# Kernel tuning notes

Measured on AMD Instinct MI355X. Metric: run time of the kernel, lower is better.

## Reference

```python
import jax, jax.numpy as jnp
import numpy as np

N_HEAD = 16


def setup_inputs() -> dict:
    key = jax.random.key(0)
    ks = jax.random.split(key, 5)
    B, T, C = 2, 2048, 1024
    s = 1.0 / np.sqrt(C)
    inp = {
        "x": jax.random.normal(ks[0], (B, T, C), dtype=jnp.float32),
        "Wq": jax.random.normal(ks[1], (C, C), dtype=jnp.float32) * s,
        "bq": jnp.zeros((C,), dtype=jnp.float32),
        "Wk": jax.random.normal(ks[2], (C, C), dtype=jnp.float32) * s,
        "bk": jnp.zeros((C,), dtype=jnp.float32),
        "Wv": jax.random.normal(ks[3], (C, C), dtype=jnp.float32) * s,
        "bv": jnp.zeros((C,), dtype=jnp.float32),
        "Wp": jax.random.normal(ks[4], (C, C), dtype=jnp.float32) * s,
        "bp": jnp.zeros((C,), dtype=jnp.float32),
    }
    return inp


def reference(x, Wq, bq, Wk, bk, Wv, bv, Wp, bp):
    B, T, C = x.shape
    H = N_HEAD
    D = C // H
    # linear projections (torch Linear: x @ W.T + b)
    q = (x @ Wq.T + bq).reshape(B, T, H, D)
    k = (x @ Wk.T + bk).reshape(B, T, H, D)
    v = (x @ Wv.T + bv).reshape(B, T, H, D)
    # scaled dot-product attention (NO causal mask in original forward)
    att = jnp.einsum("bthd,bshd->bhts", q, k) * (1.0 / np.sqrt(D))
    att = jax.nn.softmax(att, axis=-1)
    y = jnp.einsum("bhts,bshd->bthd", att, v).reshape(B, T, C)
    # output projection (dropouts are identity at p=0 / eval)
    return y @ Wp.T + bp
```

## Files before the change

### kernel.cpp

```cpp
#include <hip/hip_runtime.h>
#include <hip/hip_bf16.h>

typedef __attribute__((ext_vector_type(4))) float f32x4;
typedef __attribute__((ext_vector_type(16))) float f32x16;
typedef __attribute__((ext_vector_type(8))) short bf16x8;
typedef __attribute__((ext_vector_type(2))) unsigned int u32x2;

#define T_SEQ 2048
#define C_DIM 1024
#define NH 16
#define DHD 64

__device__ __forceinline__ unsigned cvtpk_bf16(float lo, float hi) {
    unsigned r;
    asm("v_cvt_pk_bf16_f32 %0, %1, %2" : "=v"(r) : "v"(lo), "v"(hi));
    return r;
}

__device__ __forceinline__ void async_copy16(void* lds, const void* g) {
    __builtin_amdgcn_global_load_lds(
        (const __attribute__((address_space(1))) unsigned int*)(uintptr_t)g,
        (__attribute__((address_space(3))) unsigned int*)(unsigned int)(uintptr_t)lds,
        16, 0, 0);
}

__global__ __launch_bounds__(256) void cvt_all(const float* __restrict__ x,
                                               const float* __restrict__ Wq, const float* __restrict__ Wk,
                                               const float* __restrict__ Wv, const float* __restrict__ Wp,
                                               __hip_bfloat16* __restrict__ xb,
                                               __hip_bfloat16* __restrict__ wf,
                                               __hip_bfloat16* __restrict__ wpb) {
    int i = blockIdx.x * blockDim.x + threadIdx.x;
    const float* src; __hip_bfloat16* dst; int off;
    if (i < 1048576) { src = x; dst = xb; off = i; }
    else {
        int j = i - 1048576; int wi = j >> 18; off = j & 262143;
        switch (wi) {
            case 0:  src = Wq; dst = wf;           break;
            case 1:  src = Wk; dst = wf + 1048576; break;
            case 2:  src = Wv; dst = wf + 2097152; break;
            default: src = Wp; dst = wpb;          break;
        }
    }
    float4 v = *(const float4*)(src + (size_t)off * 4);
    __hip_bfloat16 h0 = __float2bfloat16(v.x), h1 = __float2bfloat16(v.y);
    __hip_bfloat16 h2 = __float2bfloat16(v.z), h3 = __float2bfloat16(v.w);
    union { __hip_bfloat16 h[4]; u32x2 u; } p;
    p.h[0] = h0; p.h[1] = h1; p.h[2] = h2; p.h[3] = h3;
    *(u32x2*)(dst + (size_t)off * 4) = p.u;
}

__global__ __launch_bounds__(512) void gemm_qkv(const __hip_bfloat16* __restrict__ A,
                                                const __hip_bfloat16* __restrict__ Bw,
                                                const float* __restrict__ biasq,
                                                const float* __restrict__ biask,
                                                const float* __restrict__ biasv,
                                                __hip_bfloat16* __restrict__ oq,
                                                __hip_bfloat16* __restrict__ okk,
                                                __hip_bfloat16* __restrict__ ovt) {
    __shared__ __align__(16) char lds[131072];

    const int xcd = (int)blockIdx.x & 7, loc = (int)blockIdx.x >> 3;
    const int mloc = loc / 6, nloc = loc - mloc * 6;
    const int m0 = ((xcd & 3) * 4 + mloc) * 256;
    const int n0 = ((xcd >> 2) * 6 + nloc) * 256;

    const int tid = threadIdx.x;
    const int w = tid >> 6, l = tid & 63;
    const int wr = w >> 2, wc = w & 3;
    const int lg = l >> 4, lr = l & 15;

    const int sr0 = tid >> 3;
    const int sc0 = (tid & 7) * 16;
    const int gc0 = sc0 ^ ((sr0 & 7) << 4);
    const size_t goff = (size_t)sr0 * 2048 + gc0;

    const char* Ag = (const char*)A + (size_t)m0 * 2048;
    const char* Bg = (const char*)Bw + (size_t)n0 * 2048;

    auto STAGE_A = [&](int buf, int half, int kt) {
        const char* g = Ag + (size_t)(half * 128) * 2048 + kt * 128 + goff;
        char* d = lds + (buf * 2 + half) * 16384 + w * 1024;
        async_copy16(d, g);
        async_copy16(d + 8192, g + (size_t)64 * 2048);
    };
    auto STAGE_B = [&](int buf, int half, int kt) {
        const char* g = Bg + (size_t)(half * 128) * 2048 + kt * 128 + goff;
        char* d = lds + 65536 + (buf * 2 + half) * 16384 + w * 1024;
        async_copy16(d, g);
        async_copy16(d + 8192, g + (size_t)64 * 2048);
    };

    const int sw = (lr & 7) << 4;
    auto LDA = [&](bf16x8* af, int buf, int mq) {
        const char* base = lds + (buf * 2 + wr) * 16384;
        #pragma unroll
        for (int m = 0; m < 4; m++) {
            const int r = (mq * 4 + m) * 16 + lr;
            #pragma unroll
            for (int kk = 0; kk < 2; kk++)
                af[m * 2 + kk] = *(const bf16x8*)(base + r * 128 + ((kk * 64 + lg * 16) ^ sw));
        }
    };
    auto LDB = [&](bf16x8* bfv, int buf, int nq) {
        const char* base = lds + 65536 + (buf * 2 + (wc >> 1)) * 16384;
        #pragma unroll
        for (int n = 0; n < 2; n++) {
            const int r = (wc & 1) * 64 + (nq * 2 + n) * 16 + lr;
            #pragma unroll
            for (int kk = 0; kk < 2; kk++)
                bfv[n * 2 + kk] = *(const bf16x8*)(base + r * 128 + ((kk * 64 + lg * 16) ^ sw));
        }
    };

    f32x4 acc[8][4] = {};
    auto MF = [&](const bf16x8* af, const bf16x8* bfv, int mq, int nq) {
        #pragma unroll
        for (int m = 0; m < 4; m++)
            #pragma unroll
            for (int n = 0; n < 2; n++)
                #pragma unroll
                for (int kk = 0; kk < 2; kk++)
                    acc[mq * 4 + m][nq * 2 + n] = __builtin_amdgcn_mfma_f32_16x16x32_bf16(
                        af[m * 2 + kk], bfv[n * 2 + kk], acc[mq * 4 + m][nq * 2 + n], 0, 0, 0);
    };

#define PH_OPEN()  __builtin_amdgcn_sched_barrier(0); \
                   __builtin_amdgcn_s_barrier(); \
                   asm volatile("s_waitcnt lgkmcnt(0)" ::: "memory"); \
                   __builtin_amdgcn_sched_barrier(0); \
                   __builtin_amdgcn_s_setprio(1);
#define PH_CLOSE() __builtin_amdgcn_s_setprio(0); \
                   __builtin_amdgcn_sched_barrier(0); \
                   __builtin_amdgcn_s_barrier();
#define PH_CLOSE_VM() __builtin_amdgcn_s_setprio(0); \
                   asm volatile("s_waitcnt vmcnt(6)" ::: "memory"); \
                   __builtin_amdgcn_sched_barrier(0); \
                   __builtin_amdgcn_s_barrier();

    bf16x8 af[8], bf0[4], bf1[4];

    STAGE_B(0, 0, 0); STAGE_B(0, 1, 0); STAGE_A(0, 0, 0); STAGE_A(0, 1, 0);
    STAGE_B(1, 0, 1); STAGE_B(1, 1, 1); STAGE_A(1, 0, 1);
    asm volatile("s_waitcnt vmcnt(6)" ::: "memory");
    __builtin_amdgcn_sched_barrier(0);
    __builtin_amdgcn_s_barrier();

    for (int it = 0; it < 8; ++it) {
        const int t1 = 2 * it + 1;
        const int c2 = (2 * it + 2 < 16) ? 2 * it + 2 : 14;
        const int c3 = (2 * it + 3 < 16) ? 2 * it + 3 : 15;
        const int b2 = c2 & 1, b3 = c3 & 1;

        LDA(af, 0, 0); LDB(bf0, 0, 0);
        STAGE_A(1, 1, t1);
        PH_OPEN(); MF(af, bf0, 0, 0); PH_CLOSE();
        LDB(bf1, 0, 1);
        PH_OPEN(); MF(af, bf1, 0, 1); PH_CLOSE();
        LDA(af, 0, 1);
        STAGE_B(b2, 0, c2);
        PH_OPEN(); MF(af, bf1, 1, 1); PH_CLOSE();
        STAGE_B(b2, 1, c2); STAGE_A(b2, 0, c2);
        PH_OPEN(); MF(af, bf0, 1, 0); PH_CLOSE_VM();

        LDA(af, 1, 0); LDB(bf0, 1, 0);
        STAGE_A(b2, 1, c2);
        PH_OPEN(); MF(af, bf0, 0, 0); PH_CLOSE();
        LDB(bf1, 1, 1);
        PH_OPEN(); MF(af, bf1, 0, 1); PH_CLOSE();
        LDA(af, 1, 1);
        STAGE_B(b3, 0, c3);
        PH_OPEN(); MF(af, bf1, 1, 1); PH_CLOSE();
        STAGE_B(b3, 1, c3); STAGE_A(b3, 0, c3);
        PH_OPEN(); MF(af, bf0, 1, 0); PH_CLOSE_VM();
    }
#undef PH_OPEN
#undef PH_CLOSE
#undef PH_CLOSE_VM

    const int proj = n0 >> 10;
    const float* bias = (proj == 0) ? biasq : (proj == 1) ? biask : biasv;
    const float bsc = (proj == 0) ? 0.125f : 1.0f;
    #pragma unroll
    for (int m = 0; m < 8; m++)
        #pragma unroll
        for (int n = 0; n < 4; n++)
            #pragma unroll
            for (int rr = 0; rr < 4; rr++) {
                int row = m0 + wr * 128 + m * 16 + lg * 4 + rr;
                int col = n0 + wc * 64 + n * 16 + lr;
                int colL = col & (C_DIM - 1);
                float val = (acc[m][n][rr] + bias[colL]) * bsc;
                int b = row >> 11, t = row & 2047, hh = colL >> 6, dd = colL & 63;
                if (proj < 2) {
                    __hip_bfloat16* dst = (proj == 0) ? oq : okk;
                    dst[(((size_t)(b * NH + hh)) * T_SEQ + t) * DHD + dd] = __float2bfloat16(val);
                } else {
                    ovt[(((size_t)(b * NH + hh)) * DHD + dd) * T_SEQ + t] = __float2bfloat16(val);
                }
            }
}

__global__ __launch_bounds__(256) void gemm_proj(const __hip_bfloat16* __restrict__ A,
                                                 const __hip_bfloat16* __restrict__ Bw,
                                                 const float* __restrict__ biasp,
                                                 float* __restrict__ outf) {
    __shared__ __align__(16) char As[128 * 128];
    __shared__ __align__(16) char Bs[128 * 128];

    const int nwg = gridDim.x;
    const int cpx = nwg >> 3;
    const int wg = ((int)blockIdx.x & 7) * cpx + ((int)blockIdx.x >> 3);
    const int m0 = (wg & 31) * 128;
    const int n0 = (wg >> 5) * 128;

    const int tid = threadIdx.x;
    const int w = tid >> 6, l = tid & 63;
    const int wr = w >> 1, wc = w & 1;
    const int lg = l >> 4, lr = l & 15;

    const char* Ag = (const char*)A + (size_t)m0 * 2048;
    const char* Bg = (const char*)Bw + (size_t)n0 * 2048;
    const int lrow = l >> 3;
    const int scol = (l & 7) * 16;

    f32x4 acc[4][4] = {};

    for (int kt = 0; kt < 16; ++kt) {
        __syncthreads();
        #pragma unroll
        for (int i = 0; i < 4; i++) {
            const int rb = w * 32 + i * 8;
            const size_t go = (size_t)(rb + lrow) * 2048 + (size_t)kt * 128 + scol;
            async_copy16(&As[rb * 128], Ag + go);
            async_copy16(&Bs[rb * 128], Bg + go);
        }
        __syncthreads();
        #pragma unroll
        for (int kk = 0; kk < 2; kk++) {
            bf16x8 af[4], bfr[4];
            #pragma unroll
            for (int m = 0; m < 4; m++)
                af[m] = *(const bf16x8*)(&As[(wr * 64 + m * 16 + lr) * 128 + kk * 64 + lg * 16]);
            #pragma unroll
            for (int n = 0; n < 4; n++)
                bfr[n] = *(const bf16x8*)(&Bs[(wc * 64 + n * 16 + lr) * 128 + kk * 64 + lg * 16]);
            #pragma unroll
            for (int m = 0; m < 4; m++)
                #pragma unroll
                for (int n = 0; n < 4; n++)
                    acc[m][n] = __builtin_amdgcn_mfma_f32_16x16x32_bf16(af[m], bfr[n], acc[m][n], 0, 0, 0);
        }
    }

    #pragma unroll
    for (int m = 0; m < 4; m++)
        #pragma unroll
        for (int n = 0; n < 4; n++)
            #pragma unroll
            for (int r = 0; r < 4; r++) {
                int row = m0 + wr * 64 + m * 16 + lg * 4 + r;
                int col = n0 + wc * 64 + n * 16 + lr;
                outf[(size_t)row * C_DIM + col] = acc[m][n][r] + biasp[col];
            }
}

__global__ __launch_bounds__(256) void attn4(const __hip_bfloat16* __restrict__ Q,
                                             const __hip_bfloat16* __restrict__ K,
                                             const __hip_bfloat16* __restrict__ Vt,
                                             __hip_bfloat16* __restrict__ Y) {
    const int bid = blockIdx.x;
    const int xcd = bid & 7, slot = bid >> 3;
    const int head = xcd * 4 + (slot & 3);
    const int qblk = slot >> 2;

    const int tid = threadIdx.x;
    const int w = tid >> 6, l = tid & 63;
    const int lq = l & 31, hi = l >> 5;
    const int q0 = qblk * 128 + w * 32;

    __shared__ __align__(16) char Ks[3][8192];
    __shared__ __align__(16) char Vs[3][8192];
    __shared__ float bc[4][32];

    const char* Kb = (const char*)(K + (size_t)head * T_SEQ * DHD);
    const char* Vb = (const char*)(Vt + (size_t)head * DHD * T_SEQ);

    bf16x8 qf[4];
    {
        const char* qrow = (const char*)(Q + ((size_t)head * T_SEQ + q0 + lq) * DHD);
        #pragma unroll
        for (int t = 0; t < 4; t++) qf[t] = *(const bf16x8*)(qrow + t * 32 + hi * 16);
    }

    f32x16 yacc[2] = {};
    float ls0 = 0.f, ls1 = 0.f, ls2 = 0.f, ls3 = 0.f;

    const int o0 = (2 * w) * 1024 + l * 16;
    const int o1 = o0 + 1024;
    const int r0 = o0 >> 7, c0b = o0 & 127;
    const int r1 = o1 >> 7, c1b = o1 & 127;
    const int wads0 = r0 * 128 + (c0b ^ ((r0 & 7) << 4));
    const int wads1 = r1 * 128 + (c1b ^ ((r1 & 7) << 4));
    const char* vsrc0 = Vb + (size_t)r0 * (T_SEQ * 2) + c0b;
    const char* vsrc1 = Vb + (size_t)r1 * (T_SEQ * 2) + c1b;

    float4 kreg0, kreg1, vreg0, vreg1;
    auto stage_load = [&](int tile) {
        const char* kb2 = Kb + (size_t)tile * 8192;
        kreg0 = *(const float4*)(kb2 + o0);
        kreg1 = *(const float4*)(kb2 + o1);
        vreg0 = *(const float4*)(vsrc0 + (size_t)tile * 128);
        vreg1 = *(const float4*)(vsrc1 + (size_t)tile * 128);
    };
    auto stage_write = [&](int buf) {
        *(float4*)(&Ks[buf][wads0]) = kreg0;
        *(float4*)(&Ks[buf][wads1]) = kreg1;
        *(float4*)(&Vs[buf][wads0]) = vreg0;
        *(float4*)(&Vs[buf][wads1]) = vreg1;
    };

    auto qk = [&](int buf, f32x16& s0h, f32x16& s1h) {
        s0h = f32x16{}; s1h = f32x16{};
        const char* base0 = Ks[buf] + (0 * 32 + lq) * 128;
        const char* base1 = Ks[buf] + (1 * 32 + lq) * 128;
        const int sw0 = (lq & 7) << 4;
        #pragma unroll
        for (int t = 0; t < 4; t++) {
            bf16x8 kf0 = *(const bf16x8*)(base0 + ((t * 32 + hi * 16) ^ sw0));
            s0h = __builtin_amdgcn_mfma_f32_32x32x16_bf16(kf0, qf[t], s0h, 0, 0, 0);
        }
        #pragma unroll
        for (int t = 0; t < 4; t++) {
            bf16x8 kf1 = *(const bf16x8*)(base1 + ((t * 32 + hi * 16) ^ sw0));
            s1h = __builtin_amdgcn_mfma_f32_32x32x16_bf16(kf1, qf[t], s1h, 0, 0, 0);
        }
    };

    auto sm_exp = [&](f32x16& a, f32x16& b) {
        #pragma unroll
        for (int r = 0; r < 16; r += 4) {
            a[r + 0] = __expf(a[r + 0]); a[r + 1] = __expf(a[r + 1]);
            a[r + 2] = __expf(a[r + 2]); a[r + 3] = __expf(a[r + 3]);
            b[r + 0] = __expf(b[r + 0]); b[r + 1] = __expf(b[r + 1]);
            b[r + 2] = __expf(b[r + 2]); b[r + 3] = __expf(b[r + 3]);
            ls0 += a[r + 0] + b[r + 0];
            ls1 += a[r + 1] + b[r + 1];
            ls2 += a[r + 2] + b[r + 2];
            ls3 += a[r + 3] + b[r + 3];
        }
    };

    auto pv = [&](int buf, const f32x16& a, const f32x16& b) {
        unsigned pw0[8], pw1[8];
        #pragma unroll
        for (int M = 0; M < 4; M++) {
            const int u = M * 4;
            pw0[M] = cvtpk_bf16(a[u + 0], a[u + 1]);
            pw1[M] = cvtpk_bf16(a[u + 2], a[u + 3]);
            pw0[M + 4] = cvtpk_bf16(b[u + 0], b[u + 1]);
            pw1[M + 4] = cvtpk_bf16(b[u + 2], b[u + 3]);
        }
        #pragma unroll
        for (int t = 0; t < 4; t++) {
            u32x2 s0p = __builtin_amdgcn_permlane32_swap(pw0[2 * t], pw0[2 * t + 1], false, false);
            u32x2 s1p = __builtin_amdgcn_permlane32_swap(pw1[2 * t], pw1[2 * t + 1], false, false);
            union { unsigned u[4]; bf16x8 v; } af;
            af.u[0] = s0p.x; af.u[1] = s1p.x; af.u[2] = s0p.y; af.u[3] = s1p.y;
            #pragma unroll
            for (int dh = 0; dh < 2; dh++) {
                const int row = dh * 32 + lq;
                bf16x8 vf = *(const bf16x8*)(&Vs[buf][row * 128 + ((t * 32 + hi * 16) ^ ((row & 7) << 4))]);
                yacc[dh] = __builtin_amdgcn_mfma_f32_32x32x16_bf16(af.v, vf, yacc[dh], 0, 0, 0);
            }
        }
    };

    f32x16 sA0, sA1, sB0, sB1;
    stage_load(0); stage_write(0);
    stage_load(1); stage_write(1);
    stage_load(2);
    __syncthreads();
    qk(0, sA0, sA1);

    for (int t = 0; t < 32; t += 2) {
        qk((t + 1) % 3, sB0, sB1);
        if (t + 2 < 32) {
            asm volatile("s_waitcnt vmcnt(0)" ::: "memory");
            stage_write((t + 2) % 3);
            if (t + 3 < 32) stage_load(t + 3);
        }
        sm_exp(sA0, sA1);
        pv(t % 3, sA0, sA1);
        asm volatile("s_waitcnt lgkmcnt(0)" ::: "memory");
        __builtin_amdgcn_s_barrier();
        __builtin_amdgcn_sched_barrier(0);
        const int t1 = t + 1;
        if (t1 + 1 < 32) qk((t1 + 1) % 3, sA0, sA1);
        if (t1 + 2 < 32) {
            asm volatile("s_waitcnt vmcnt(0)" ::: "memory");
            stage_write((t1 + 2) % 3);
            if (t1 + 3 < 32) stage_load(t1 + 3);
        }
        sm_exp(sB0, sB1);
        pv(t1 % 3, sB0, sB1);
        asm volatile("s_waitcnt lgkmcnt(0)" ::: "memory");
        __builtin_amdgcn_s_barrier();
        __builtin_amdgcn_sched_barrier(0);
    }

    float lsum = (ls0 + ls1) + (ls2 + ls3);
    lsum += __shfl_xor(lsum, 32);
    float inv = 1.0f / lsum;
    if (hi == 0) bc[w][lq] = inv;
    asm volatile("s_waitcnt lgkmcnt(0)" ::: "memory");
    __builtin_amdgcn_sched_barrier(0);

    const int b = head >> 4, h16 = head & 15;
    const size_t rowbase = (size_t)b * T_SEQ + q0;
    #pragma unroll
    for (int r = 0; r < 16; r++) {
        const int crow = (r & 3) + 8 * (r >> 2) + 4 * hi;
        const float iv = bc[w][crow];
        const size_t row = rowbase + crow;
        Y[row * C_DIM + h16 * DHD + lq]      = __float2bfloat16(yacc[0][r] * iv);
        Y[row * C_DIM + h16 * DHD + 32 + lq] = __float2bfloat16(yacc[1][r] * iv);
    }
}

extern "C" void kernel_launch(void* const* d_in, const int* in_sizes, int n_in,
                              void* d_out, int out_size, void* d_ws, size_t ws_size,
                              hipStream_t stream) {
    (void)in_sizes; (void)n_in; (void)out_size; (void)ws_size;
    const float* x  = (const float*)d_in[0];
    const float* Wq = (const float*)d_in[1];
    const float* bq = (const float*)d_in[2];
    const float* Wk = (const float*)d_in[3];
    const float* bk = (const float*)d_in[4];
    const float* Wv = (const float*)d_in[5];
    const float* bv = (const float*)d_in[6];
    const float* Wp = (const float*)d_in[7];
    const float* bp = (const float*)d_in[8];
    float* out = (float*)d_out;

    char* ws = (char*)d_ws;
    const size_t MC = (size_t)4096 * C_DIM;
    const size_t CC = (size_t)C_DIM * C_DIM;
    __hip_bfloat16* xb  = (__hip_bfloat16*)ws;  ws += MC * 2;
    __hip_bfloat16* wf  = (__hip_bfloat16*)ws;  ws += 3 * CC * 2;
    __hip_bfloat16* wpb = (__hip_bfloat16*)ws;  ws += CC * 2;
    __hip_bfloat16* qb  = (__hip_bfloat16*)ws;  ws += MC * 2;
    __hip_bfloat16* kb  = (__hip_bfloat16*)ws;  ws += MC * 2;
    __hip_bfloat16* vtb = (__hip_bfloat16*)ws;  ws += MC * 2;
    __hip_bfloat16* yb  = (__hip_bfloat16*)ws;  ws += MC * 2;

    cvt_all<<<8192, 256, 0, stream>>>(x, Wq, Wk, Wv, Wp, xb, wf, wpb);

    gemm_qkv<<<192, 512, 0, stream>>>(xb, wf, bq, bk, bv, qb, kb, vtb);

    attn4<<<512, 256, 0, stream>>>(qb, kb, vtb, yb);

    gemm_proj<<<256, 256, 0, stream>>>(yb, wpb, bp, out);
}
```

Before: 140.2 us.

## Load V fragments directly from global, fold log2e into Q, vectorize Vt stores

The attention kernel no longer stages V tiles through LDS. Each lane reads its V fragments straight from global memory inside the PV step, which removes the V LDS writes and reads but puts global load latency inside the compute loop with no prefetch. The Q scale now includes log2(e), so the softmax can use the hardware exp2 instruction in place of __expf. The QKV GEMM epilogue also packs four bf16 values per store when writing transposed V.

Measured after the change: 138.7 us. No clear change (-1.1%).

```diff
diff --git a/kernel.cpp b/kernel.cpp
--- a/kernel.cpp
+++ b/kernel.cpp
@@ -14,6 +14,12 @@
 __device__ __forceinline__ unsigned cvtpk_bf16(float lo, float hi) {
     unsigned r;
     asm("v_cvt_pk_bf16_f32 %0, %1, %2" : "=v"(r) : "v"(lo), "v"(hi));
+    return r;
+}
+
+__device__ __forceinline__ float exp2_hw(float x) {
+    float r;
+    asm("v_exp_f32 %0, %1" : "=v"(r) : "v"(x));
     return r;
 }
 
@@ -43,10 +49,9 @@
         }
     }
     float4 v = *(const float4*)(src + (size_t)off * 4);
-    __hip_bfloat16 h0 = __float2bfloat16(v.x), h1 = __float2bfloat16(v.y);
-    __hip_bfloat16 h2 = __float2bfloat16(v.z), h3 = __float2bfloat16(v.w);
     union { __hip_bfloat16 h[4]; u32x2 u; } p;
-    p.h[0] = h0; p.h[1] = h1; p.h[2] = h2; p.h[3] = h3;
+    p.h[0] = __float2bfloat16(v.x); p.h[1] = __float2bfloat16(v.y);
+    p.h[2] = __float2bfloat16(v.z); p.h[3] = __float2bfloat16(v.w);
     *(u32x2*)(dst + (size_t)off * 4) = p.u;
 }
 
@@ -179,26 +184,42 @@
 #undef PH_CLOSE_VM
 
     const int proj = n0 >> 10;
-    const float* bias = (proj == 0) ? biasq : (proj == 1) ? biask : biasv;
-    const float bsc = (proj == 0) ? 0.125f : 1.0f;
-    #pragma unroll
-    for (int m = 0; m < 8; m++)
-        #pragma unroll
-        for (int n = 0; n < 4; n++)
-            #pragma unroll
-            for (int rr = 0; rr < 4; rr++) {
-                int row = m0 + wr * 128 + m * 16 + lg * 4 + rr;
+    if (proj < 2) {
+        const float* bias = (proj == 0) ? biasq : biask;
+        const float bsc = (proj == 0) ? 0.125f * 1.4426950408889634f : 1.0f;
+        __hip_bfloat16* dst = (proj == 0) ? oq : okk;
+        #pragma unroll
+        for (int m = 0; m < 8; m++)
+            #pragma unroll
+            for (int n = 0; n < 4; n++)
+                #pragma unroll
+                for (int rr = 0; rr < 4; rr++) {
+                    int row = m0 + wr * 128 + m * 16 + lg * 4 + rr;
+                    int col = n0 + wc * 64 + n * 16 + lr;
+                    int colL = col & (C_DIM - 1);
+                    float val = (acc[m][n][rr] + bias[colL]) * bsc;
+                    int b = row >> 11, t = row & 2047, hh = colL >> 6, dd = colL & 63;
+                    dst[(((size_t)(b * NH + hh)) * T_SEQ + t) * DHD + dd] = __float2bfloat16(val);
+                }
+    } else {
+        #pragma unroll
+        for (int m = 0; m < 8; m++) {
+            const int rowb = m0 + wr * 128 + m * 16 + lg * 4;
+            const int b = rowb >> 11, t0 = rowb & 2047;
+            #pragma unroll
+            for (int n = 0; n < 4; n++) {
                 int col = n0 + wc * 64 + n * 16 + lr;
                 int colL = col & (C_DIM - 1);
-                float val = (acc[m][n][rr] + bias[colL]) * bsc;
-                int b = row >> 11, t = row & 2047, hh = colL >> 6, dd = colL & 63;
-                if (proj < 2) {
-                    __hip_bfloat16* dst = (proj == 0) ? oq : okk;
-                    dst[(((size_t)(b * NH + hh)) * T_SEQ + t) * DHD + dd] = __float2bfloat16(val);
-                } else {
-                    ovt[(((size_t)(b * NH + hh)) * DHD + dd) * T_SEQ + t] = __float2bfloat16(val);
-                }
+                int hh = colL >> 6, dd = colL & 63;
+                float bv = biasv[colL];
+                union { __hip_bfloat16 h[4]; u32x2 u; } p;
+                #pragma unroll
+                for (int rr = 0; rr < 4; rr++)
+                    p.h[rr] = __float2bfloat16(acc[m][n][rr] + bv);
+                *(u32x2*)&ovt[(((size_t)(b * NH + hh)) * DHD + dd) * T_SEQ + t0] = p.u;
             }
+        }
+    }
 }
 
 __global__ __launch_bounds__(256) void gemm_proj(const __hip_bfloat16* __restrict__ A,
@@ -265,7 +286,7 @@
             }
 }
 
-__global__ __launch_bounds__(256) void attn4(const __hip_bfloat16* __restrict__ Q,
+__global__ __launch_bounds__(256) void attn5(const __hip_bfloat16* __restrict__ Q,
                                              const __hip_bfloat16* __restrict__ K,
                                              const __hip_bfloat16* __restrict__ Vt,
                                              __hip_bfloat16* __restrict__ Y) {
@@ -280,7 +301,6 @@
     const int q0 = qblk * 128 + w * 32;
 
     __shared__ __align__(16) char Ks[3][8192];
-    __shared__ __align__(16) char Vs[3][8192];
     __shared__ float bc[4][32];
 
     const char* Kb = (const char*)(K + (size_t)head * T_SEQ * DHD);
@@ -302,22 +322,16 @@
     const int r1 = o1 >> 7, c1b = o1 & 127;
     const int wads0 = r0 * 128 + (c0b ^ ((r0 & 7) << 4));
     const int wads1 = r1 * 128 + (c1b ^ ((r1 & 7) << 4));
-    const char* vsrc0 = Vb + (size_t)r0 * (T_SEQ * 2) + c0b;
-    const char* vsrc1 = Vb + (size_t)r1 * (T_SEQ * 2) + c1b;
-
-    float4 kreg0, kreg1, vreg0, vreg1;
+
+    float4 kreg0, kreg1;
     auto stage_load = [&](int tile) {
         const char* kb2 = Kb + (size_t)tile * 8192;
         kreg0 = *(const float4*)(kb2 + o0);
         kreg1 = *(const float4*)(kb2 + o1);
-        vreg0 = *(const float4*)(vsrc0 + (size_t)tile * 128);
-        vreg1 = *(const float4*)(vsrc1 + (size_t)tile * 128);
     };
     auto stage_write = [&](int buf) {
         *(float4*)(&Ks[buf][wads0]) = kreg0;
         *(float4*)(&Ks[buf][wads1]) = kreg1;
-        *(float4*)(&Vs[buf][wads0]) = vreg0;
-        *(float4*)(&Vs[buf][wads1]) = vreg1;
     };
 
     auto qk = [&](int buf, f32x16& s0h, f32x16& s1h) {
@@ -340,10 +354,10 @@
     auto sm_exp = [&](f32x16& a, f32x16& b) {
         #pragma unroll
         for (int r = 0; r < 16; r += 4) {
-            a[r + 0] = __expf(a[r + 0]); a[r + 1] = __expf(a[r + 1]);
-            a[r + 2] = __expf(a[r + 2]); a[r + 3] = __expf(a[r + 3]);
-            b[r + 0] = __expf(b[r + 0]); b[r + 1] = __expf(b[r + 1]);
-            b[r + 2] = __expf(b[r + 2]); b[r + 3] = __expf(b[r + 3]);
+            a[r + 0] = exp2_hw(a[r + 0]); a[r + 1] = exp2_hw(a[r + 1]);
+            a[r + 2] = exp2_hw(a[r + 2]); a[r + 3] = exp2_hw(a[r + 3]);
+            b[r + 0] = exp2_hw(b[r + 0]); b[r + 1] = exp2_hw(b[r + 1]);
+            b[r + 2] = exp2_hw(b[r + 2]); b[r + 3] = exp2_hw(b[r + 3]);
             ls0 += a[r + 0] + b[r + 0];
             ls1 += a[r + 1] + b[r + 1];
             ls2 += a[r + 2] + b[r + 2];
@@ -351,7 +365,14 @@
         }
     };
 
-    auto pv = [&](int buf, const f32x16& a, const f32x16& b) {
+    auto pv = [&](int tile, const f32x16& a, const f32x16& b) {
+        bf16x8 vf[8];
+        const char* vb = Vb + (size_t)tile * 128;
+        #pragma unroll
+        for (int t = 0; t < 4; t++)
+            #pragma unroll
+            for (int dh = 0; dh < 2; dh++)
+                vf[t * 2 + dh] = *(const bf16x8*)(vb + (size_t)(dh * 32 + lq) * (T_SEQ * 2) + t * 32 + hi * 16);
         unsigned pw0[8], pw1[8];
         #pragma unroll
         for (int M = 0; M < 4; M++) {
@@ -368,11 +389,8 @@
             union { unsigned u[4]; bf16x8 v; } af;
             af.u[0] = s0p.x; af.u[1] = s1p.x; af.u[2] = s0p.y; af.u[3] = s1p.y;
             #pragma unroll
-            for (int dh = 0; dh < 2; dh++) {
-                const int row = dh * 32 + lq;
-                bf16x8 vf = *(const bf16x8*)(&Vs[buf][row * 128 + ((t * 32 + hi * 16) ^ ((row & 7) << 4))]);
-                yacc[dh] = __builtin_amdgcn_mfma_f32_32x32x16_bf16(af.v, vf, yacc[dh], 0, 0, 0);
-            }
+            for (int dh = 0; dh < 2; dh++)
+                yacc[dh] = __builtin_amdgcn_mfma_f32_32x32x16_bf16(af.v, vf[t * 2 + dh], yacc[dh], 0, 0, 0);
         }
     };
 
@@ -391,10 +409,11 @@
             if (t + 3 < 32) stage_load(t + 3);
         }
         sm_exp(sA0, sA1);
-        pv(t % 3, sA0, sA1);
+        pv(t, sA0, sA1);
         asm volatile("s_waitcnt lgkmcnt(0)" ::: "memory");
         __builtin_amdgcn_s_barrier();
         __builtin_amdgcn_sched_barrier(0);
+
         const int t1 = t + 1;
         if (t1 + 1 < 32) qk((t1 + 1) % 3, sA0, sA1);
         if (t1 + 2 < 32) {
@@ -403,7 +422,7 @@
             if (t1 + 3 < 32) stage_load(t1 + 3);
         }
         sm_exp(sB0, sB1);
-        pv(t1 % 3, sB0, sB1);
+        pv(t1, sB0, sB1);
         asm volatile("s_waitcnt lgkmcnt(0)" ::: "memory");
         __builtin_amdgcn_s_barrier();
         __builtin_amdgcn_sched_barrier(0);
@@ -458,7 +477,7 @@
 
     gemm_qkv<<<192, 512, 0, stream>>>(xb, wf, bq, bk, bv, qb, kb, vtb);
 
-    attn4<<<512, 256, 0, stream>>>(qb, kb, vtb, yb);
+    attn5<<<512, 256, 0, stream>>>(qb, kb, vtb, yb);
 
     gemm_proj<<<256, 256, 0, stream>>>(yb, wpb, bp, out);
 }
```
